# Kernel optimization log

Hardware: AMD Instinct MI355X
Metric: run time of the kernel (lower is better)

## Reference

```python
import jax, jax.numpy as jnp
import numpy as np

N_ITEMS = 100000
N_EDGES = 800000
D = 64
N_LAYERS = 3  # config['ii_layers']


def setup_inputs() -> dict:
    key = jax.random.key(0)
    k1, k2, k3, k4 = jax.random.split(key, 4)
    rows = jax.random.randint(k1, (N_EDGES,), 0, N_ITEMS, dtype=jnp.int64 if jax.config.jax_enable_x64 else jnp.int32)
    cols = jax.random.randint(k2, (N_EDGES,), 0, N_ITEMS, dtype=jnp.int64 if jax.config.jax_enable_x64 else jnp.int32)
    vals = jax.random.uniform(k3, (N_EDGES,), dtype=jnp.float32)
    item_embeddings = jax.random.normal(k4, (N_ITEMS, D), dtype=jnp.float32)
    return {"rows": rows, "cols": cols, "vals": vals, "item_embeddings": item_embeddings}


def _spmm(rows, cols, vals, x):
    # sparse.mm(A, x) with A in COO: out[r] += vals[e] * x[c] for each edge e=(r,c)
    msgs = vals[:, None] * x[cols]            # [E, D] gathered & weighted messages
    return jax.ops.segment_sum(msgs, rows, num_segments=N_ITEMS)


def reference(rows, cols, vals, item_embeddings):
    # HyperConv: iterate SpMM, average initial + all layer outputs (fused running sum).
    acc = item_embeddings
    cur = item_embeddings
    for _ in range(N_LAYERS):
        cur = _spmm(rows, cols, vals, cur)
        acc = acc + cur
    return acc / jnp.asarray(N_LAYERS + 1, dtype=item_embeddings.dtype)
```

## Files before the change

kernel.cpp:

```cpp
#include <hip/hip_runtime.h>
#include <hip/hip_fp16.h>


#define NI 100000
#define NE 800000
#define DD 64

#define RPB   512
#define BINS  ((NI + RPB - 1) / RPB)
#define EPB   2048
#define P1B   ((NE + EPB - 1) / EPB)
#define CAP   5120
#define BC    32
#define CVB   6250
#define SPLIT 4
#define RQ    (RPB / SPLIT)
#define NTILE (NI / 32)

typedef int   i4 __attribute__((ext_vector_type(4)));
typedef float f4 __attribute__((ext_vector_type(4)));

static __device__ __forceinline__ float2 h2f(int w) {
    __half2 h = *(__half2*)&w;
    return __half22float2(h);
}

static __device__ __forceinline__ void spmm_tile(int vb, int mode,
                                                 const int* __restrict__ fill,
                                                 const int2* __restrict__ bucket,
                                                 const __half* __restrict__ xin,
                                                 __half* __restrict__ nxt,
                                                 const float* __restrict__ x0,
                                                 const __half* __restrict__ s1,
                                                 float* __restrict__ outp) {
    int tid  = threadIdx.x;
    int lane = tid & 63;
    int grp  = lane >> 3;
    int ll   = lane & 7;
    int r    = vb * 32 + (tid >> 6) * 8 + grp;
    int deg  = fill[r];
    const int2* ep = bucket + (size_t)r * BC;

    int wmax = deg;
    wmax = max(wmax, __shfl_xor(wmax, 8, 64));
    wmax = max(wmax, __shfl_xor(wmax, 16, 64));
    wmax = max(wmax, __shfl_xor(wmax, 32, 64));
    int wmax4 = (wmax + 3) & ~3;

    i4 q0 = (i4)0, q1 = (i4)0;
    if (2 * ll < deg)      q0 = __builtin_nontemporal_load((const i4*)(ep + 2 * ll));
    if (16 + 2 * ll < deg) q1 = __builtin_nontemporal_load((const i4*)(ep + 16 + 2 * ll));

    float a0 = 0.f, a1 = 0.f, a2 = 0.f, a3 = 0.f;
    float a4 = 0.f, a5 = 0.f, a6 = 0.f, a7 = 0.f;

    for (int j = 0; j < wmax4; j += 4) {
        int s0 = (lane & 56) | ((j >> 1) & 7);
        int s1i = s0 + 1;
        i4 qa = (j < 16) ? q0 : q1;
        int c0  = __shfl(qa[0], s0, 64);
        int v0i = __shfl(qa[1], s0, 64);
        int c1  = __shfl(qa[2], s0, 64);
        int v1i = __shfl(qa[3], s0, 64);
        int c2  = __shfl(qa[0], s1i, 64);
        int v2i = __shfl(qa[1], s1i, 64);
        int c3  = __shfl(qa[2], s1i, 64);
        int v3i = __shfl(qa[3], s1i, 64);

        i4 g0 = *(const i4*)(xin + (size_t)c0 * DD + 8 * ll);
        i4 g1 = *(const i4*)(xin + (size_t)c1 * DD + 8 * ll);
        i4 g2 = *(const i4*)(xin + (size_t)c2 * DD + 8 * ll);
        i4 g3 = *(const i4*)(xin + (size_t)c3 * DD + 8 * ll);

        float v0 = __int_as_float(v0i);
        float v1 = __int_as_float(v1i);
        float v2 = __int_as_float(v2i);
        float v3 = __int_as_float(v3i);
        float2 f;
        f = h2f(g0[0]); a0 += v0 * f.x; a1 += v0 * f.y;
        f = h2f(g0[1]); a2 += v0 * f.x; a3 += v0 * f.y;
        f = h2f(g0[2]); a4 += v0 * f.x; a5 += v0 * f.y;
        f = h2f(g0[3]); a6 += v0 * f.x; a7 += v0 * f.y;
        f = h2f(g1[0]); a0 += v1 * f.x; a1 += v1 * f.y;
        f = h2f(g1[1]); a2 += v1 * f.x; a3 += v1 * f.y;
        f = h2f(g1[2]); a4 += v1 * f.x; a5 += v1 * f.y;
        f = h2f(g1[3]); a6 += v1 * f.x; a7 += v1 * f.y;
        f = h2f(g2[0]); a0 += v2 * f.x; a1 += v2 * f.y;
        f = h2f(g2[1]); a2 += v2 * f.x; a3 += v2 * f.y;
        f = h2f(g2[2]); a4 += v2 * f.x; a5 += v2 * f.y;
        f = h2f(g2[3]); a6 += v2 * f.x; a7 += v2 * f.y;
        f = h2f(g3[0]); a0 += v3 * f.x; a1 += v3 * f.y;
        f = h2f(g3[1]); a2 += v3 * f.x; a3 += v3 * f.y;
        f = h2f(g3[2]); a4 += v3 * f.x; a5 += v3 * f.y;
        f = h2f(g3[3]); a6 += v3 * f.x; a7 += v3 * f.y;
    }

    if (mode == 2) {
        size_t fo = (size_t)r * DD + 8 * ll;
        f4 xa = __builtin_nontemporal_load((const f4*)(x0 + fo));
        f4 xb = __builtin_nontemporal_load((const f4*)(x0 + fo) + 1);
        i4 s1u = __builtin_nontemporal_load((const i4*)(s1 + fo));
        i4 s2u = *(const i4*)(xin + fo);
        f4 oa, ob;
        float2 f1, f2;
        f1 = h2f(s1u[0]); f2 = h2f(s2u[0]);
        oa[0] = (xa[0] + f1.x + f2.x + a0) * 0.25f;
        oa[1] = (xa[1] + f1.y + f2.y + a1) * 0.25f;
        f1 = h2f(s1u[1]); f2 = h2f(s2u[1]);
        oa[2] = (xa[2] + f1.x + f2.x + a2) * 0.25f;
        oa[3] = (xa[3] + f1.y + f2.y + a3) * 0.25f;
        f1 = h2f(s1u[2]); f2 = h2f(s2u[2]);
        ob[0] = (xb[0] + f1.x + f2.x + a4) * 0.25f;
        ob[1] = (xb[1] + f1.y + f2.y + a5) * 0.25f;
        f1 = h2f(s1u[3]); f2 = h2f(s2u[3]);
        ob[2] = (xb[2] + f1.x + f2.x + a6) * 0.25f;
        ob[3] = (xb[3] + f1.y + f2.y + a7) * 0.25f;
        f4* op = (f4*)(outp + fo);
        __builtin_nontemporal_store(oa, op);
        __builtin_nontemporal_store(ob, op + 1);
    } else {
        i4 o;
        __half2 h;
        h = __floats2half2_rn(a0, a1); o[0] = *(int*)&h;
        h = __floats2half2_rn(a2, a3); o[1] = *(int*)&h;
        h = __floats2half2_rn(a4, a5); o[2] = *(int*)&h;
        h = __floats2half2_rn(a6, a7); o[3] = *(int*)&h;
        *(i4*)(nxt + (size_t)r * DD + 8 * ll) = o;
    }
}

__global__ __launch_bounds__(256) void part1_conv_k(const int* __restrict__ rows,
                                                    const int* __restrict__ cols,
                                                    const float* __restrict__ vals,
                                                    int* __restrict__ bin_cnt,
                                                    int2* __restrict__ binned,
                                                    const float4* __restrict__ x,
                                                    __half* __restrict__ xh,
                                                    int n4) {
    int t = threadIdx.x;
    if (blockIdx.x >= P1B) {
        int i = (blockIdx.x - P1B) * 256 + t;
        if (i < n4) {
            float4 v = x[i];
            __half2* dst = (__half2*)(xh + (size_t)i * 4);
            dst[0] = __floats2half2_rn(v.x, v.y);
            dst[1] = __floats2half2_rn(v.z, v.w);
        }
        return;
    }

    __shared__ int  hist[BINS];
    __shared__ int  offs[BINS];
    __shared__ int  base[BINS];
    __shared__ int  cur[BINS];
    __shared__ int  sc[256];
    __shared__ int2 stage[EPB];
    __shared__ unsigned char sbin[EPB];

    int e0   = blockIdx.x * EPB;
    int ecnt = NE - e0; if (ecnt > EPB) ecnt = EPB;

    for (int i = t; i < BINS; i += 256) { hist[i] = 0; cur[i] = 0; }
    __syncthreads();
    for (int i = t; i < ecnt; i += 256)
        atomicAdd(&hist[rows[e0 + i] >> 9], 1);
    __syncthreads();

    int hv = (t < BINS) ? hist[t] : 0;
    sc[t] = hv;
    __syncthreads();
    for (int off = 1; off < 256; off <<= 1) {
        int xv = (t >= off) ? sc[t - off] : 0;
        __syncthreads();
        sc[t] += xv;
        __syncthreads();
    }
    if (t < BINS) {
        offs[t] = sc[t] - hv;
        base[t] = hv ? atomicAdd(&bin_cnt[t], hv) : 0;
    }
    __syncthreads();

    for (int i = t; i < ecnt; i += 256) {
        int r = rows[e0 + i];
        int b = r >> 9;
        int p = offs[b] + atomicAdd(&cur[b], 1);
        stage[p] = make_int2(((r & 511) << 17) | cols[e0 + i],
                             __float_as_int(vals[e0 + i]));
        sbin[p] = (unsigned char)b;
    }
    __syncthreads();

    for (int i = t; i < ecnt; i += 256) {
        int b   = sbin[i];
        int pos = base[b] + (i - offs[b]);
        if (pos < CAP) binned[(size_t)b * CAP + pos] = stage[i];
    }
}

__global__ __launch_bounds__(256, 8) void p2s0_k(const int* __restrict__ bin_cnt,
                                                 const int2* __restrict__ binned,
                                                 int2* __restrict__ bucket,
                                                 int* __restrict__ fill,
                                                 const __half* __restrict__ xh,
                                                 __half* __restrict__ s1h) {
    __shared__ int cur[RQ];
    int t  = threadIdx.x;
    int bb = blockIdx.x >> 2;
    int q  = blockIdx.x & 3;
    for (int i = t; i < RQ; i += 256) cur[i] = 0;
    __syncthreads();
    int cnt = bin_cnt[bb];
    if (cnt > CAP) cnt = CAP;
    const int2* src = binned + (size_t)bb * CAP;
    for (int i = t; i < cnt; i += 256) {
        int2 e = src[i];
        int rl = e.x >> 17;
        if ((rl >> 7) == q) {
            int pos = atomicAdd(&cur[rl & (RQ - 1)], 1);
            if (pos < BC)
                bucket[((size_t)bb * RPB + rl) * BC + pos] =
                    make_int2(e.x & 0x1FFFF, e.y);
        }
    }
    __syncthreads();
    for (int i = t; i < RQ; i += 256) {
        int rl = q * RQ + i;
        int r  = bb * RPB + rl;
        if (r < NI) {
            int c = (cur[i] < BC) ? cur[i] : BC;
            if (c & 1) {
                bucket[((size_t)bb * RPB + rl) * BC + c] = make_int2(0, 0);
                c++;
            }
            fill[r] = c;
        }
    }
    __syncthreads();

    int vb0 = bb * 16 + q * 4;
    for (int s = 0; s < 4; ++s) {
        int vb = vb0 + s;
        if (vb < NTILE)
            spmm_tile(vb, 0, fill, bucket, xh, s1h, nullptr, nullptr, nullptr);
    }
}

template <int MODE>
__global__ __launch_bounds__(256, 8) void spmm_k(const int* __restrict__ fill,
                                                 const int2* __restrict__ bucket,
                                                 const __half* __restrict__ xin,
                                                 __half* __restrict__ nxt,
                                                 const float* __restrict__ x0,
                                                 const __half* __restrict__ s1,
                                                 float* __restrict__ outp) {
    spmm_tile(blockIdx.x, MODE, fill, bucket, xin, nxt, x0, s1, outp);
}

#define NB ((NI + 255) / 256)

__global__ __launch_bounds__(256) void init_k(const float4* __restrict__ x,
                                              float4* __restrict__ cur,
                                              float4* __restrict__ acc, int n4) {
    int i = blockIdx.x * 256 + threadIdx.x;
    if (i < n4) { float4 v = x[i]; cur[i] = v; acc[i] = v; }
}

__global__ __launch_bounds__(256) void hist_k(const int* __restrict__ rows,
                                              int* __restrict__ counts) {
    int e = blockIdx.x * 256 + threadIdx.x;
    if (e < NE) atomicAdd(&counts[rows[e]], 1);
}

__global__ __launch_bounds__(256) void scan1_k(const int* __restrict__ counts,
                                               int* __restrict__ bsum) {
    __shared__ int s[256];
    int t = threadIdx.x;
    int i = blockIdx.x * 256 + t;
    s[t] = (i < NI) ? counts[i] : 0;
    __syncthreads();
    for (int off = 128; off > 0; off >>= 1) {
        if (t < off) s[t] += s[t + off];
        __syncthreads();
    }
    if (t == 0) bsum[blockIdx.x] = s[0];
}

__global__ __launch_bounds__(512) void scan2_k(int* __restrict__ bsum) {
    __shared__ int s[512];
    int t = threadIdx.x;
    int v = (t < NB) ? bsum[t] : 0;
    s[t] = v;
    __syncthreads();
    for (int off = 1; off < 512; off <<= 1) {
        int tmp = (t >= off) ? s[t - off] : 0;
        __syncthreads();
        s[t] += tmp;
        __syncthreads();
    }
    if (t < NB) bsum[t] = s[t] - v;
}

__global__ __launch_bounds__(256) void scan3_k(const int* __restrict__ counts,
                                               const int* __restrict__ bsum,
                                               int* __restrict__ rowptr) {
    __shared__ int s[256];
    int t = threadIdx.x;
    int i = blockIdx.x * 256 + t;
    int v = (i < NI) ? counts[i] : 0;
    s[t] = v;
    __syncthreads();
    for (int off = 1; off < 256; off <<= 1) {
        int tmp = (t >= off) ? s[t - off] : 0;
        __syncthreads();
        s[t] += tmp;
        __syncthreads();
    }
    int excl = s[t] - v + bsum[blockIdx.x];
    if (i < NI) rowptr[i] = excl;
    if (i == NI - 1) rowptr[NI] = excl + v;
}

__global__ __launch_bounds__(256) void scatter_k(const int* __restrict__ rows,
                                                 const int* __restrict__ cols,
                                                 const float* __restrict__ vals,
                                                 const int* __restrict__ rowptr,
                                                 int* __restrict__ fillc,
                                                 int2* __restrict__ edges) {
    int e = blockIdx.x * 256 + threadIdx.x;
    if (e < NE) {
        int r = rows[e];
        int pos = rowptr[r] + atomicAdd(&fillc[r], 1);
        edges[pos] = make_int2(cols[e], __float_as_int(vals[e]));
    }
}

__global__ __launch_bounds__(256) void spmm_csr_k(const int* __restrict__ rowptr,
                                                  const int2* __restrict__ edges,
                                                  const float* __restrict__ x,
                                                  float* __restrict__ nxt,
                                                  float* __restrict__ acc,
                                                  int last) {
    int r = __builtin_amdgcn_readfirstlane(blockIdx.x * 4 + (threadIdx.x >> 6));
    int lane = threadIdx.x & 63;
    int beg = rowptr[r];
    int end = rowptr[r + 1];
    float s = 0.f;
    int j = beg;
    for (; j + 3 < end; j += 4) {
        int2 e0 = edges[j], e1 = edges[j + 1], e2 = edges[j + 2], e3 = edges[j + 3];
        float g0 = x[(size_t)e0.x * DD + lane];
        float g1 = x[(size_t)e1.x * DD + lane];
        float g2 = x[(size_t)e2.x * DD + lane];
        float g3 = x[(size_t)e3.x * DD + lane];
        s += __int_as_float(e0.y) * g0; s += __int_as_float(e1.y) * g1;
        s += __int_as_float(e2.y) * g2; s += __int_as_float(e3.y) * g3;
    }
    for (; j < end; ++j) {
        int2 e = edges[j];
        s += __int_as_float(e.y) * x[(size_t)e.x * DD + lane];
    }
    size_t o = (size_t)r * DD + lane;
    if (last) acc[o] = (acc[o] + s) * 0.25f;
    else { nxt[o] = s; acc[o] += s; }
}

extern "C" void kernel_launch(void* const* d_in, const int* in_sizes, int n_in,
                              void* d_out, int out_size, void* d_ws, size_t ws_size,
                              hipStream_t stream) {
    const int*   rows = (const int*)d_in[0];
    const int*   cols = (const int*)d_in[1];
    const float* vals = (const float*)d_in[2];
    const float* x    = (const float*)d_in[3];
    float* outp = (float*)d_out;

    const size_t fbuf  = (size_t)NI * DD * sizeof(float);
    const size_t hbuf  = (size_t)NI * DD * sizeof(__half);
    const int    n4        = NI * DD / 4;
    const int    grid_elem = (n4 + 255) / 256;

    char* wsp = (char*)d_ws;

    size_t off_xh     = 0;
    size_t off_s1     = off_xh + hbuf;
    size_t off_s2     = off_s1 + hbuf;
    size_t off_bucket = off_s2 + hbuf;
    size_t off_binned = off_bucket + (size_t)NI * BC * 8;
    size_t off_fill   = off_binned + (size_t)BINS * CAP * 8;
    size_t off_bcnt   = off_fill + (size_t)NI * 4;
    size_t need       = off_bcnt + (size_t)BINS * 4;

    if (ws_size >= need) {
        __half* xh      = (__half*)(wsp + off_xh);
        __half* s1h     = (__half*)(wsp + off_s1);
        __half* s2h     = (__half*)(wsp + off_s2);
        int2*   bucket  = (int2*)(wsp + off_bucket);
        int2*   binned  = (int2*)(wsp + off_binned);
        int*    fill    = (int*)(wsp + off_fill);
        int*    bin_cnt = (int*)(wsp + off_bcnt);

        hipMemsetAsync(bin_cnt, 0, BINS * sizeof(int), stream);
        part1_conv_k<<<P1B + CVB, 256, 0, stream>>>(rows, cols, vals, bin_cnt, binned,
                                                    (const float4*)x, xh, n4);
        p2s0_k<<<BINS * SPLIT, 256, 0, stream>>>(bin_cnt, binned, bucket, fill,
                                                 xh, s1h);
        spmm_k<1><<<NTILE, 256, 0, stream>>>(fill, bucket, s1h, s2h, nullptr, nullptr, nullptr);
        spmm_k<2><<<NTILE, 256, 0, stream>>>(fill, bucket, s2h, nullptr, x, s1h, outp);
        return;
    }

    const int grid_edge = (NE + 255) / 256;
    const int grid_csr  = NI / 4;

    float* bufA   = (float*)wsp;
    float* bufB   = (float*)(wsp + fbuf);
    int2*  edges  = (int2*)(wsp + 2 * fbuf);
    int*   rowptr = (int*)(wsp + 2 * fbuf + (size_t)NE * 8);
    int*   counts = rowptr + (NI + 1);
    int*   bsum   = counts + NI;

    hipMemsetAsync(counts, 0, NI * sizeof(int), stream);
    hist_k<<<grid_edge, 256, 0, stream>>>(rows, counts);
    scan1_k<<<NB, 256, 0, stream>>>(counts, bsum);
    scan2_k<<<1, 512, 0, stream>>>(bsum);
    scan3_k<<<NB, 256, 0, stream>>>(counts, bsum, rowptr);
    hipMemsetAsync(counts, 0, NI * sizeof(int), stream);
    scatter_k<<<grid_edge, 256, 0, stream>>>(rows, cols, vals, rowptr, counts, edges);
    init_k<<<grid_elem, 256, 0, stream>>>((const float4*)x, (float4*)bufA,
                                          (float4*)outp, n4);
    spmm_csr_k<<<grid_csr, 256, 0, stream>>>(rowptr, edges, bufA, bufB, outp, 0);
    spmm_csr_k<<<grid_csr, 256, 0, stream>>>(rowptr, edges, bufB, bufA, outp, 0);
    spmm_csr_k<<<grid_csr, 256, 0, stream>>>(rowptr, edges, bufA, bufB, outp, 1);
}
```

Before: 173.2 us.

## Replace global-atomic capped bins with per-block bin segments and prefix-search gather

The edge binning stage no longer reserves slots in a fixed-capacity global bin array through global atomics. Each partition block now writes its locally sorted edges contiguously, along with per-bin counts and offsets. The second stage rebuilds each bin by prefix-scanning those counts across all partition blocks and binary-searching to gather the edges, which removes the capacity cap and the memset. The first SpMM layer, previously fused into the bucketing kernel, now runs as its own launch, adding one kernel launch and a per-edge binary search in exchange.

```diff
diff --git a/kernel.cpp b/kernel.cpp
--- a/kernel.cpp
+++ b/kernel.cpp
@@ -10,7 +10,6 @@
 #define BINS  ((NI + RPB - 1) / RPB)
 #define EPB   2048
 #define P1B   ((NE + EPB - 1) / EPB)
-#define CAP   5120
 #define BC    32
 #define CVB   6250
 #define SPLIT 4
@@ -132,8 +131,9 @@
 __global__ __launch_bounds__(256) void part1_conv_k(const int* __restrict__ rows,
                                                     const int* __restrict__ cols,
                                                     const float* __restrict__ vals,
-                                                    int* __restrict__ bin_cnt,
-                                                    int2* __restrict__ binned,
+                                                    int* __restrict__ cnts_g,
+                                                    int* __restrict__ offs_g,
+                                                    int2* __restrict__ binned2,
                                                     const float4* __restrict__ x,
                                                     __half* __restrict__ xh,
                                                     int n4) {
@@ -151,7 +151,6 @@
 
     __shared__ int  hist[BINS];
     __shared__ int  offs[BINS];
-    __shared__ int  base[BINS];
     __shared__ int  cur[BINS];
     __shared__ int  sc[256];
     __shared__ int2 stage[EPB];
@@ -175,10 +174,7 @@
         sc[t] += xv;
         __syncthreads();
     }
-    if (t < BINS) {
-        offs[t] = sc[t] - hv;
-        base[t] = hv ? atomicAdd(&bin_cnt[t], hv) : 0;
-    }
+    if (t < BINS) offs[t] = sc[t] - hv;
     __syncthreads();
 
     for (int i = t; i < ecnt; i += 256) {
@@ -191,30 +187,59 @@
     }
     __syncthreads();
 
-    for (int i = t; i < ecnt; i += 256) {
-        int b   = sbin[i];
-        int pos = base[b] + (i - offs[b]);
-        if (pos < CAP) binned[(size_t)b * CAP + pos] = stage[i];
-    }
-}
-
-__global__ __launch_bounds__(256, 8) void p2s0_k(const int* __restrict__ bin_cnt,
-                                                 const int2* __restrict__ binned,
-                                                 int2* __restrict__ bucket,
-                                                 int* __restrict__ fill,
-                                                 const __half* __restrict__ xh,
-                                                 __half* __restrict__ s1h) {
+    for (int i = t; i < ecnt; i += 256)
+        binned2[(size_t)blockIdx.x * EPB + i] = stage[i];
+    if (t < BINS) {
+        cnts_g[blockIdx.x * BINS + t] = hist[t];
+        offs_g[blockIdx.x * BINS + t] = offs[t];
+    }
+    (void)sbin;
+}
+
+__global__ __launch_bounds__(256) void part2_k(const int* __restrict__ cnts_g,
+                                               const int* __restrict__ offs_g,
+                                               const int2* __restrict__ binned2,
+                                               int2* __restrict__ bucket,
+                                               int* __restrict__ fill) {
+    __shared__ int cntl[P1B];
+    __shared__ int ofl[P1B];
+    __shared__ int pfx[P1B + 1];
+    __shared__ int sc[256];
     __shared__ int cur[RQ];
     int t  = threadIdx.x;
     int bb = blockIdx.x >> 2;
     int q  = blockIdx.x & 3;
+
+    for (int blk = t; blk < P1B; blk += 256) {
+        cntl[blk] = cnts_g[blk * BINS + bb];
+        ofl[blk]  = offs_g[blk * BINS + bb];
+    }
     for (int i = t; i < RQ; i += 256) cur[i] = 0;
     __syncthreads();
-    int cnt = bin_cnt[bb];
-    if (cnt > CAP) cnt = CAP;
-    const int2* src = binned + (size_t)bb * CAP;
-    for (int i = t; i < cnt; i += 256) {
-        int2 e = src[i];
+
+    int c0 = (2 * t < P1B)     ? cntl[2 * t]     : 0;
+    int c1 = (2 * t + 1 < P1B) ? cntl[2 * t + 1] : 0;
+    sc[t] = c0 + c1;
+    __syncthreads();
+    for (int off = 1; off < 256; off <<= 1) {
+        int xv = (t >= off) ? sc[t - off] : 0;
+        __syncthreads();
+        sc[t] += xv;
+        __syncthreads();
+    }
+    int excl = sc[t] - (c0 + c1);
+    if (2 * t     <= P1B) pfx[2 * t]     = excl;
+    if (2 * t + 1 <= P1B) pfx[2 * t + 1] = excl + c0;
+    __syncthreads();
+    int total = pfx[P1B];
+
+    for (int g = t; g < total; g += 256) {
+        int lo = 0, hi = P1B - 1;
+        while (lo < hi) {
+            int mid = (lo + hi + 1) >> 1;
+            if (pfx[mid] <= g) lo = mid; else hi = mid - 1;
+        }
+        int2 e = binned2[(size_t)lo * EPB + ofl[lo] + (g - pfx[lo])];
         int rl = e.x >> 17;
         if ((rl >> 7) == q) {
             int pos = atomicAdd(&cur[rl & (RQ - 1)], 1);
@@ -235,14 +260,6 @@
             }
             fill[r] = c;
         }
-    }
-    __syncthreads();
-
-    int vb0 = bb * 16 + q * 4;
-    for (int s = 0; s < 4; ++s) {
-        int vb = vb0 + s;
-        if (vb < NTILE)
-            spmm_tile(vb, 0, fill, bucket, xh, s1h, nullptr, nullptr, nullptr);
     }
 }
 
@@ -385,25 +402,26 @@
     size_t off_s1     = off_xh + hbuf;
     size_t off_s2     = off_s1 + hbuf;
     size_t off_bucket = off_s2 + hbuf;
-    size_t off_binned = off_bucket + (size_t)NI * BC * 8;
-    size_t off_fill   = off_binned + (size_t)BINS * CAP * 8;
-    size_t off_bcnt   = off_fill + (size_t)NI * 4;
-    size_t need       = off_bcnt + (size_t)BINS * 4;
+    size_t off_b2     = off_bucket + (size_t)NI * BC * 8;
+    size_t off_cnts   = off_b2 + (size_t)P1B * EPB * 8;
+    size_t off_offs   = off_cnts + (size_t)P1B * BINS * 4;
+    size_t off_fill   = off_offs + (size_t)P1B * BINS * 4;
+    size_t need       = off_fill + (size_t)NI * 4;
 
     if (ws_size >= need) {
         __half* xh      = (__half*)(wsp + off_xh);
         __half* s1h     = (__half*)(wsp + off_s1);
         __half* s2h     = (__half*)(wsp + off_s2);
         int2*   bucket  = (int2*)(wsp + off_bucket);
-        int2*   binned  = (int2*)(wsp + off_binned);
+        int2*   binned2 = (int2*)(wsp + off_b2);
+        int*    cnts_g  = (int*)(wsp + off_cnts);
+        int*    offs_g  = (int*)(wsp + off_offs);
         int*    fill    = (int*)(wsp + off_fill);
-        int*    bin_cnt = (int*)(wsp + off_bcnt);
-
-        hipMemsetAsync(bin_cnt, 0, BINS * sizeof(int), stream);
-        part1_conv_k<<<P1B + CVB, 256, 0, stream>>>(rows, cols, vals, bin_cnt, binned,
-                                                    (const float4*)x, xh, n4);
-        p2s0_k<<<BINS * SPLIT, 256, 0, stream>>>(bin_cnt, binned, bucket, fill,
-                                                 xh, s1h);
+
+        part1_conv_k<<<P1B + CVB, 256, 0, stream>>>(rows, cols, vals, cnts_g, offs_g,
+                                                    binned2, (const float4*)x, xh, n4);
+        part2_k<<<BINS * SPLIT, 256, 0, stream>>>(cnts_g, offs_g, binned2, bucket, fill);
+        spmm_k<0><<<NTILE, 256, 0, stream>>>(fill, bucket, xh,  s1h, nullptr, nullptr, nullptr);
         spmm_k<1><<<NTILE, 256, 0, stream>>>(fill, bucket, s1h, s2h, nullptr, nullptr, nullptr);
         spmm_k<2><<<NTILE, 256, 0, stream>>>(fill, bucket, s2h, nullptr, x, s1h, outp);
         return;
```

After: 179.3 us. 3.5% more time.
